# Kernel optimization log

Hardware: AMD Instinct MI355X
Metric: run time of the kernel (lower is better)

Reference implementation:

```python
import jax, jax.numpy as jnp
import numpy as np


def setup_inputs() -> dict:
    key = jax.random.key(0)
    k1, k2 = jax.random.split(key)
    B, N, D = 32, 8192, 64
    x = jax.random.normal(k1, (B, N, D), dtype=jnp.float32)
    y = jax.random.normal(k2, (B, D, N), dtype=jnp.float32)
    return {"x": x, "y": y}


def reference(x, y):
    # Original: full cdist [B,N,N], mean over batch, take diagonal.
    # Only matched pairs (i,i) survive, so compute them directly —
    # mathematically identical output and gradients.
    y_t = jnp.transpose(y, (0, 2, 1))          # [B, N, D]
    diff = x - y_t                             # [B, N, D]
    pair_dist = jnp.sqrt(jnp.sum(diff * diff, axis=-1))  # [B, N]
    dist_diag = jnp.mean(pair_dist, axis=0)    # [N] == diag(mean_b cdist)
    dist_diag = dist_diag.at[1:3].multiply(1.5)
    loss = jnp.mean(dist_diag)
    return loss
```

## Files before the change

kernel.cpp:

```cpp
#include <hip/hip_runtime.h>


constexpr int B  = 32;
constexpr int N  = 8192;
constexpr int D  = 64;
constexpr int TN = 128;
constexpr int NBLK = (N / TN) * B;

__global__ __launch_bounds__(256) void euclid_loss_kernel(
    const float* __restrict__ x,
    const float* __restrict__ y,
    float* __restrict__ ws)
{
    const int tid = threadIdx.x;
    const int w   = tid >> 6;
    const int g   = tid & 63;
    const int c   = g & 15;
    const int dw  = g >> 4;
    const int nh  = w >> 1;
    const int dh  = w & 1;
    const int n0  = blockIdx.x * TN;
    const int b   = blockIdx.y;
    const int nb  = n0 + nh * 64 + 4 * c;
    const int d0  = dh * 32 + dw * 8;

    const float* xp = x + ((size_t)b * N + nb) * D + d0;
    const float* yp = y + ((size_t)b * D + d0) * N + nb;

    float4 xr[4][2];
#pragma unroll
    for (int r = 0; r < 4; ++r) {
        xr[r][0] = *reinterpret_cast<const float4*>(xp + r * D + 0);
        xr[r][1] = *reinterpret_cast<const float4*>(xp + r * D + 4);
    }
    float4 yv[8];
#pragma unroll
    for (int jd = 0; jd < 8; ++jd)
        yv[jd] = *reinterpret_cast<const float4*>(yp + (size_t)jd * N);

    float acc[4] = {0.f, 0.f, 0.f, 0.f};
#define ACC_R(r, CMP)                                          \
    { float t;                                                 \
      t = xr[r][0].x - yv[0].CMP; acc[r] += t * t;             \
      t = xr[r][0].y - yv[1].CMP; acc[r] += t * t;             \
      t = xr[r][0].z - yv[2].CMP; acc[r] += t * t;             \
      t = xr[r][0].w - yv[3].CMP; acc[r] += t * t;             \
      t = xr[r][1].x - yv[4].CMP; acc[r] += t * t;             \
      t = xr[r][1].y - yv[5].CMP; acc[r] += t * t;             \
      t = xr[r][1].z - yv[6].CMP; acc[r] += t * t;             \
      t = xr[r][1].w - yv[7].CMP; acc[r] += t * t; }
    ACC_R(0, x)
    ACC_R(1, y)
    ACC_R(2, z)
    ACC_R(3, w)
#undef ACC_R

    __shared__ float partF[2][4][128];
    *reinterpret_cast<float4*>(&partF[dh][dw][nh * 64 + 4 * c]) =
        make_float4(acc[0], acc[1], acc[2], acc[3]);
    __syncthreads();

    float v = 0.f;
    if (tid < TN) {
        const int nh2 = tid >> 6;
        const int m   = tid & 63;
        float s = 0.f;
#pragma unroll
        for (int dh2 = 0; dh2 < 2; ++dh2)
#pragma unroll
            for (int dw2 = 0; dw2 < 4; ++dw2)
                s += partF[dh2][dw2][nh2 * 64 + m];
        const int n = n0 + tid;
        const float wt = (n == 1 || n == 2) ? 1.5f : 1.0f;
        v = wt * __builtin_sqrtf(s);
    }
#pragma unroll
    for (int off = 32; off > 0; off >>= 1) v += __shfl_down(v, off, 64);

    __shared__ float wsum[4];
    if ((tid & 63) == 0) wsum[tid >> 6] = v;
    __syncthreads();
    if (tid == 0)
        ws[blockIdx.y * gridDim.x + blockIdx.x] =
            wsum[0] + wsum[1] + wsum[2] + wsum[3];
}

__global__ __launch_bounds__(256) void reduce_kernel(
    const float* __restrict__ ws,
    float* __restrict__ out)
{
    const int tid = threadIdx.x;
    float v = 0.f;
#pragma unroll
    for (int j = 0; j < NBLK / (256 * 4); ++j) {
        const float4 p = *reinterpret_cast<const float4*>(ws + j * 1024 + tid * 4);
        v += p.x + p.y + p.z + p.w;
    }
#pragma unroll
    for (int off = 32; off > 0; off >>= 1) v += __shfl_down(v, off, 64);

    __shared__ float wsum[4];
    if ((tid & 63) == 0) wsum[tid >> 6] = v;
    __syncthreads();
    if (tid == 0)
        out[0] = (wsum[0] + wsum[1] + wsum[2] + wsum[3]) * (1.0f / (float)(B * N));
}

extern "C" void kernel_launch(void* const* d_in, const int* in_sizes, int n_in,
                              void* d_out, int out_size, void* d_ws, size_t ws_size,
                              hipStream_t stream) {
    const float* x = (const float*)d_in[0];
    const float* y = (const float*)d_in[1];
    float* out = (float*)d_out;
    float* ws  = (float*)d_ws;

    dim3 grid(N / TN, B);
    euclid_loss_kernel<<<grid, 256, 0, stream>>>(x, y, ws);
    reduce_kernel<<<1, 256, 0, stream>>>(ws, out);
}
```

Before: 141.7 us.

## Process four batches per block with double-buffered register loads

Measured after the change: 141.8 us. No clear change (+0.1%).

```diff
diff --git a/kernel.cpp b/kernel.cpp
--- a/kernel.cpp
+++ b/kernel.cpp
@@ -5,7 +5,9 @@
 constexpr int N  = 8192;
 constexpr int D  = 64;
 constexpr int TN = 128;
-constexpr int NBLK = (N / TN) * B;
+constexpr int GX = N / TN;
+constexpr int GY = 8;
+constexpr int NBLK = B * GX;
 
 __global__ __launch_bounds__(256) void euclid_loss_kernel(
     const float* __restrict__ x,
@@ -20,69 +22,105 @@
     const int nh  = w >> 1;
     const int dh  = w & 1;
     const int n0  = blockIdx.x * TN;
-    const int b   = blockIdx.y;
+    const int by  = blockIdx.y;
     const int nb  = n0 + nh * 64 + 4 * c;
     const int d0  = dh * 32 + dw * 8;
 
-    const float* xp = x + ((size_t)b * N + nb) * D + d0;
-    const float* yp = y + ((size_t)b * D + d0) * N + nb;
+    const float* xb = x + ((size_t)by * N + nb) * D + d0;
+    const float* yb = y + ((size_t)by * D + d0) * N + nb;
+    constexpr size_t TS = (size_t)GY * N * D;
 
-    float4 xr[4][2];
+    float4 xrA[4][2], xrB[4][2], yvA[8], yvB[8];
+    float  accT[4][4];
 #pragma unroll
-    for (int r = 0; r < 4; ++r) {
-        xr[r][0] = *reinterpret_cast<const float4*>(xp + r * D + 0);
-        xr[r][1] = *reinterpret_cast<const float4*>(xp + r * D + 4);
+    for (int t = 0; t < 4; ++t)
+#pragma unroll
+        for (int r = 0; r < 4; ++r) accT[t][r] = 0.f;
+
+#define LOADT(XR, YV, t)                                                        \
+    {                                                                           \
+        const float* xpt = xb + (size_t)(t) * TS;                               \
+        const float* ypt = yb + (size_t)(t) * TS;                               \
+        _Pragma("unroll")                                                       \
+        for (int r = 0; r < 4; ++r) {                                           \
+            XR[r][0] = *reinterpret_cast<const float4*>(xpt + r * D);           \
+            XR[r][1] = *reinterpret_cast<const float4*>(xpt + r * D + 4);       \
+        }                                                                       \
+        _Pragma("unroll")                                                       \
+        for (int jd = 0; jd < 8; ++jd)                                          \
+            YV[jd] = *reinterpret_cast<const float4*>(ypt + (size_t)jd * N);    \
     }
-    float4 yv[8];
+
+#define ACC1(XR, YV, acc, r, CMP)                                               \
+    { float t_;                                                                 \
+      t_ = XR[r][0].x - YV[0].CMP; acc[r] += t_ * t_;                           \
+      t_ = XR[r][0].y - YV[1].CMP; acc[r] += t_ * t_;                           \
+      t_ = XR[r][0].z - YV[2].CMP; acc[r] += t_ * t_;                           \
+      t_ = XR[r][0].w - YV[3].CMP; acc[r] += t_ * t_;                           \
+      t_ = XR[r][1].x - YV[4].CMP; acc[r] += t_ * t_;                           \
+      t_ = XR[r][1].y - YV[5].CMP; acc[r] += t_ * t_;                           \
+      t_ = XR[r][1].z - YV[6].CMP; acc[r] += t_ * t_;                           \
+      t_ = XR[r][1].w - YV[7].CMP; acc[r] += t_ * t_; }
+
+#define CONSUME(XR, YV, acc)                                                    \
+    ACC1(XR, YV, acc, 0, x) ACC1(XR, YV, acc, 1, y)                             \
+    ACC1(XR, YV, acc, 2, z) ACC1(XR, YV, acc, 3, w)
+
+    LOADT(xrA, yvA, 0)
+    LOADT(xrB, yvB, 1)
+    CONSUME(xrA, yvA, accT[0])
+    LOADT(xrA, yvA, 2)
+    CONSUME(xrB, yvB, accT[1])
+    LOADT(xrB, yvB, 3)
+    CONSUME(xrA, yvA, accT[2])
+    CONSUME(xrB, yvB, accT[3])
+
+#undef LOADT
+#undef ACC1
+#undef CONSUME
+
+    __shared__ float partF[4][2][4][128];
 #pragma unroll
-    for (int jd = 0; jd < 8; ++jd)
-        yv[jd] = *reinterpret_cast<const float4*>(yp + (size_t)jd * N);
-
-    float acc[4] = {0.f, 0.f, 0.f, 0.f};
-#define ACC_R(r, CMP)                                          \
-    { float t;                                                 \
-      t = xr[r][0].x - yv[0].CMP; acc[r] += t * t;             \
-      t = xr[r][0].y - yv[1].CMP; acc[r] += t * t;             \
-      t = xr[r][0].z - yv[2].CMP; acc[r] += t * t;             \
-      t = xr[r][0].w - yv[3].CMP; acc[r] += t * t;             \
-      t = xr[r][1].x - yv[4].CMP; acc[r] += t * t;             \
-      t = xr[r][1].y - yv[5].CMP; acc[r] += t * t;             \
-      t = xr[r][1].z - yv[6].CMP; acc[r] += t * t;             \
-      t = xr[r][1].w - yv[7].CMP; acc[r] += t * t; }
-    ACC_R(0, x)
-    ACC_R(1, y)
-    ACC_R(2, z)
-    ACC_R(3, w)
-#undef ACC_R
-
-    __shared__ float partF[2][4][128];
-    *reinterpret_cast<float4*>(&partF[dh][dw][nh * 64 + 4 * c]) =
-        make_float4(acc[0], acc[1], acc[2], acc[3]);
+    for (int t = 0; t < 4; ++t)
+        *reinterpret_cast<float4*>(&partF[t][dh][dw][nh * 64 + 4 * c]) =
+            make_float4(accT[t][0], accT[t][1], accT[t][2], accT[t][3]);
     __syncthreads();
 
-    float v = 0.f;
+    float v0 = 0.f, v1 = 0.f, v2 = 0.f, v3 = 0.f;
     if (tid < TN) {
         const int nh2 = tid >> 6;
         const int m   = tid & 63;
-        float s = 0.f;
+        float s0 = 0.f, s1 = 0.f, s2 = 0.f, s3 = 0.f;
 #pragma unroll
         for (int dh2 = 0; dh2 < 2; ++dh2)
 #pragma unroll
-            for (int dw2 = 0; dw2 < 4; ++dw2)
-                s += partF[dh2][dw2][nh2 * 64 + m];
+            for (int dw2 = 0; dw2 < 4; ++dw2) {
+                s0 += partF[0][dh2][dw2][nh2 * 64 + m];
+                s1 += partF[1][dh2][dw2][nh2 * 64 + m];
+                s2 += partF[2][dh2][dw2][nh2 * 64 + m];
+                s3 += partF[3][dh2][dw2][nh2 * 64 + m];
+            }
         const int n = n0 + tid;
         const float wt = (n == 1 || n == 2) ? 1.5f : 1.0f;
-        v = wt * __builtin_sqrtf(s);
+        v0 = wt * __builtin_sqrtf(s0);
+        v1 = wt * __builtin_sqrtf(s1);
+        v2 = wt * __builtin_sqrtf(s2);
+        v3 = wt * __builtin_sqrtf(s3);
     }
 #pragma unroll
-    for (int off = 32; off > 0; off >>= 1) v += __shfl_down(v, off, 64);
-
-    __shared__ float wsum[4];
-    if ((tid & 63) == 0) wsum[tid >> 6] = v;
+    for (int off = 32; off > 0; off >>= 1) {
+        v0 += __shfl_down(v0, off, 64);
+        v1 += __shfl_down(v1, off, 64);
+        v2 += __shfl_down(v2, off, 64);
+        v3 += __shfl_down(v3, off, 64);
+    }
+    __shared__ float wsum[2][4];
+    if (g == 0 && w < 2) {
+        wsum[w][0] = v0; wsum[w][1] = v1; wsum[w][2] = v2; wsum[w][3] = v3;
+    }
     __syncthreads();
-    if (tid == 0)
-        ws[blockIdx.y * gridDim.x + blockIdx.x] =
-            wsum[0] + wsum[1] + wsum[2] + wsum[3];
+    if (tid < 4)
+        ws[(by + 8 * tid) * GX + blockIdx.x] = wsum[0][tid] + wsum[1][tid];
 }
 
 __global__ __launch_bounds__(256) void reduce_kernel(
@@ -114,7 +152,7 @@
     float* out = (float*)d_out;
     float* ws  = (float*)d_ws;
 
-    dim3 grid(N / TN, B);
+    dim3 grid(GX, GY);
     euclid_loss_kernel<<<grid, 256, 0, stream>>>(x, y, ws);
     reduce_kernel<<<1, 256, 0, stream>>>(ws, out);
 }
```
